# Performance work log

Measured on AMD Instinct MI355X. Metric: run time of the kernel, lower is better.

Reference implementation:

```python
import jax, jax.numpy as jnp
import numpy as np

LAMBDA = 0.01  # sparsity_threshold
SCALE = 0.02
NUM_BLOCKS = 4


def setup_inputs() -> dict:
    key = jax.random.key(0)
    k1, k2, k3, k4, k5 = jax.random.split(key, 5)
    B, N, C = 8, 4096, 512
    bs = C // NUM_BLOCKS
    return {
        "x": jax.random.normal(k1, (B, N, C), dtype=jnp.float32),
        "w1": jax.random.normal(k2, (2, NUM_BLOCKS, bs, bs), dtype=jnp.float32) * SCALE,
        "w2": jax.random.normal(k3, (2, NUM_BLOCKS, bs, bs), dtype=jnp.float32) * SCALE,
        "b1": jax.random.normal(k4, (2, NUM_BLOCKS, bs), dtype=jnp.float32) * SCALE,
        "b2": jax.random.normal(k5, (2, NUM_BLOCKS, bs), dtype=jnp.float32) * SCALE,
        "H": 64,
        "W": 64,
    }


def _softshrink(v):
    return jnp.where(v > LAMBDA, v - LAMBDA, jnp.where(v < -LAMBDA, v + LAMBDA, jnp.zeros((), v.dtype)))


def reference(x, w1, w2, b1, b2, H, W):
    B, N, C = x.shape
    bs = C // NUM_BLOCKS
    xb = x.reshape(B, N, NUM_BLOCKS, bs)
    # FFT over (token, block) axes, ortho norm — faithful to torch fft2(dim=(1,2))
    xf = jnp.fft.fft2(xb, axes=(1, 2), norm="ortho")
    re, im = jnp.real(xf), jnp.imag(xf)

    mul = lambda a, w: jnp.einsum("tnbd,bdk->tnbk", a, w)  # block-diagonal matmul

    r1 = jax.nn.relu(mul(re, w1[0]) - mul(im, w1[1]) + b1[0])
    i1 = jax.nn.relu(mul(re, w1[1]) + mul(im, w1[0]) + b1[1])
    r2 = mul(r1, w2[0]) - mul(i1, w2[1]) + b2[0]
    i2 = mul(r1, w2[1]) + mul(i1, w2[0]) + b2[1]

    z = _softshrink(r2) + 1j * _softshrink(i2)
    out = jnp.real(jnp.fft.ifft2(z, axes=(1, 2), norm="ortho"))  # .to(float32) keeps real part
    return out.reshape(B, N, C).astype(jnp.float32)
```

## Files before the change

### kernel.cpp

```cpp
#include <hip/hip_runtime.h>
#include <math.h>

#define TWO_PI 6.283185307179586f

typedef __attribute__((ext_vector_type(8))) short bf16x8;
typedef __attribute__((ext_vector_type(4))) short bf16x4;
typedef __attribute__((ext_vector_type(4))) float f32x4;
typedef __attribute__((ext_vector_type(4))) _Float16 h16x4;
typedef __attribute__((ext_vector_type(8))) _Float16 h16x8;

__device__ __forceinline__ short f2bf(float f) {
    unsigned u = __float_as_uint(f);
    unsigned r = (u + 0x7FFFu + ((u >> 16) & 1u)) >> 16;
    return (short)r;
}
__device__ __forceinline__ float bf2f(short s) {
    return __uint_as_float(((unsigned)(unsigned short)s) << 16);
}

__device__ __forceinline__ int dr4(int s) {
    return ((s & 3) << 4) | (s & 12) | ((s >> 4) & 3);
}

__device__ __forceinline__ void cmulw(float& xr, float& xi, float wr, float wi) {
    const float tr = xr * wr - xi * wi;
    xi = xr * wi + xi * wr;
    xr = tr;
}

template<int W>
__device__ __forceinline__ void fft64_dif4v(_Float16 (*Lre)[W], _Float16 (*Lim)[W],
                                            const float* wtr, const float* wti,
                                            int c4, int h) {
#pragma unroll
    for (int s = 0; s < 3; ++s) {
        const int q  = 16 >> (2 * s);
        const int tw = 1 << (2 * s);
        __syncthreads();
        const int j = h & (q - 1);
        const int g = (s == 0) ? 0 : (h >> (4 - 2 * s));
        const int i0 = g * (q << 2) + j;
        const int i1 = i0 + q, i2 = i1 + q, i3 = i2 + q;
        const h16x4 A0r = *(const h16x4*)&Lre[i0][c4], A0i = *(const h16x4*)&Lim[i0][c4];
        const h16x4 A1r = *(const h16x4*)&Lre[i1][c4], A1i = *(const h16x4*)&Lim[i1][c4];
        const h16x4 A2r = *(const h16x4*)&Lre[i2][c4], A2i = *(const h16x4*)&Lim[i2][c4];
        const h16x4 A3r = *(const h16x4*)&Lre[i3][c4], A3i = *(const h16x4*)&Lim[i3][c4];
        const int m = j * tw;
        const float w1r = wtr[m],     w1i = wti[m];
        const float w2r = wtr[2 * m], w2i = wti[2 * m];
        const float w3r = wtr[3 * m], w3i = wti[3 * m];
        h16x4 O0r, O0i, O1r, O1i, O2r, O2i, O3r, O3i;
#pragma unroll
        for (int e = 0; e < 4; ++e) {
            const float a0r = (float)A0r[e], a0i = (float)A0i[e];
            const float a1r = (float)A1r[e], a1i = (float)A1i[e];
            const float a2r = (float)A2r[e], a2i = (float)A2i[e];
            const float a3r = (float)A3r[e], a3i = (float)A3i[e];
            const float t0r = a0r + a2r, t0i = a0i + a2i;
            const float t2r = a0r - a2r, t2i = a0i - a2i;
            const float t1r = a1r + a3r, t1i = a1i + a3i;
            const float dr  = a1r - a3r, di  = a1i - a3i;
            const float t3r = di, t3i = -dr;
            O0r[e] = (_Float16)(t0r + t1r);  O0i[e] = (_Float16)(t0i + t1i);
            float y1r = t2r + t3r, y1i = t2i + t3i;
            float y2r = t0r - t1r, y2i = t0i - t1i;
            float y3r = t2r - t3r, y3i = t2i - t3i;
            if (m) {
                cmulw(y1r, y1i, w1r, w1i);
                cmulw(y2r, y2i, w2r, w2i);
                cmulw(y3r, y3i, w3r, w3i);
            }
            O1r[e] = (_Float16)y1r; O1i[e] = (_Float16)y1i;
            O2r[e] = (_Float16)y2r; O2i[e] = (_Float16)y2i;
            O3r[e] = (_Float16)y3r; O3i[e] = (_Float16)y3i;
        }
        *(h16x4*)&Lre[i0][c4] = O0r;  *(h16x4*)&Lim[i0][c4] = O0i;
        *(h16x4*)&Lre[i1][c4] = O1r;  *(h16x4*)&Lim[i1][c4] = O1i;
        *(h16x4*)&Lre[i2][c4] = O2r;  *(h16x4*)&Lim[i2][c4] = O2i;
        *(h16x4*)&Lre[i3][c4] = O3r;  *(h16x4*)&Lim[i3][c4] = O3i;
    }
    __syncthreads();
}

template<int W>
__device__ __forceinline__ void fft64_dit4v(_Float16 (*Lre)[W], _Float16 (*Lim)[W],
                                            const float* wtr, const float* wti,
                                            int c4, int h) {
#pragma unroll
    for (int s = 2; s >= 0; --s) {
        const int q  = 16 >> (2 * s);
        const int tw = 1 << (2 * s);
        __syncthreads();
        const int j = h & (q - 1);
        const int g = (s == 0) ? 0 : (h >> (4 - 2 * s));
        const int i0 = g * (q << 2) + j;
        const int i1 = i0 + q, i2 = i1 + q, i3 = i2 + q;
        const h16x4 A0r = *(const h16x4*)&Lre[i0][c4], A0i = *(const h16x4*)&Lim[i0][c4];
        const h16x4 A1r = *(const h16x4*)&Lre[i1][c4], A1i = *(const h16x4*)&Lim[i1][c4];
        const h16x4 A2r = *(const h16x4*)&Lre[i2][c4], A2i = *(const h16x4*)&Lim[i2][c4];
        const h16x4 A3r = *(const h16x4*)&Lre[i3][c4], A3i = *(const h16x4*)&Lim[i3][c4];
        const int m = j * tw;
        const float w1r = wtr[m],     w1i = -wti[m];
        const float w2r = wtr[2 * m], w2i = -wti[2 * m];
        const float w3r = wtr[3 * m], w3i = -wti[3 * m];
        h16x4 O0r, O0i, O1r, O1i, O2r, O2i, O3r, O3i;
#pragma unroll
        for (int e = 0; e < 4; ++e) {
            float b1r = (float)A1r[e], b1i = (float)A1i[e];
            float b2r = (float)A2r[e], b2i = (float)A2i[e];
            float b3r = (float)A3r[e], b3i = (float)A3i[e];
            if (m) {
                cmulw(b1r, b1i, w1r, w1i);
                cmulw(b2r, b2i, w2r, w2i);
                cmulw(b3r, b3i, w3r, w3i);
            }
            const float a0r = (float)A0r[e], a0i = (float)A0i[e];
            const float u0r = a0r + b2r, u0i = a0i + b2i;
            const float u1r = a0r - b2r, u1i = a0i - b2i;
            const float u2r = b1r + b3r, u2i = b1i + b3i;
            const float dr  = b1r - b3r, di  = b1i - b3i;
            const float u3r = -di, u3i = dr;
            O0r[e] = (_Float16)(u0r + u2r); O0i[e] = (_Float16)(u0i + u2i);
            O1r[e] = (_Float16)(u1r + u3r); O1i[e] = (_Float16)(u1i + u3i);
            O2r[e] = (_Float16)(u0r - u2r); O2i[e] = (_Float16)(u0i - u2i);
            O3r[e] = (_Float16)(u1r - u3r); O3i[e] = (_Float16)(u1i - u3i);
        }
        *(h16x4*)&Lre[i0][c4] = O0r;  *(h16x4*)&Lim[i0][c4] = O0i;
        *(h16x4*)&Lre[i1][c4] = O1r;  *(h16x4*)&Lim[i1][c4] = O1i;
        *(h16x4*)&Lre[i2][c4] = O2r;  *(h16x4*)&Lim[i2][c4] = O2i;
        *(h16x4*)&Lre[i3][c4] = O3r;  *(h16x4*)&Lim[i3][c4] = O3i;
    }
    __syncthreads();
}

#define DECODE_BCT() \
    const int b  = blockIdx.x >> 8; \
    const int dg = (blockIdx.x >> 2) & 63; \
    const int ct = blockIdx.x & 3;

#define GADDR(slot, blk, f4) \
    (((size_t)(b * 4096 + (slot)) * 512) + (size_t)((blk) * 128 + ct * 32 + (f4) * 4))

#define GADDR8(slot, blk, e8) \
    (((size_t)(b * 4096 + (slot)) * 512) + (size_t)((blk) * 128 + ct * 32 + (e8) * 8))

#define SETUP_TABLE48() \
    if (tid < 48) { \
        float s_, c_; \
        sincosf(TWO_PI * (float)tid / 64.0f, &s_, &c_); \
        wre[tid] = c_; wim[tid] = -s_; \
    }

extern "C" __global__ void __launch_bounds__(512)
fft_fwd_a(const float* __restrict__ x, short* __restrict__ zre, short* __restrict__ zim) {
    __shared__ __align__(16) _Float16 Lre[64][136];
    __shared__ __align__(16) _Float16 Lim[64][136];
    __shared__ float wre[48], wim[48];
    __shared__ float twr[64], twi[64];
    const int tid = threadIdx.x;
    SETUP_TABLE48();
    DECODE_BCT();
    if (tid >= 64 && tid < 128) {
        const int s1 = tid - 64;
        float sn, cs;
        sincosf(-(TWO_PI / 4096.0f) * (float)(dg * dr4(s1)), &sn, &cs);
        twr[s1] = cs; twi[s1] = sn;
    }
    for (int idx = tid; idx < 2048; idx += 512) {
        const int n1 = idx >> 5, q = idx & 31, blk = q >> 3, f4 = q & 7;
        const int cl = blk * 32 + f4 * 4;
        const float4 v = *(const float4*)(x + GADDR(n1 * 64 + dg, blk, f4));
        h16x4 hv, hz;
        hv[0] = (_Float16)v.x; hv[1] = (_Float16)v.y;
        hv[2] = (_Float16)v.z; hv[3] = (_Float16)v.w;
        hz[0] = (_Float16)0.f; hz[1] = (_Float16)0.f;
        hz[2] = (_Float16)0.f; hz[3] = (_Float16)0.f;
        *(h16x4*)&Lre[n1][cl] = hv;
        *(h16x4*)&Lim[n1][cl] = hz;
    }
    fft64_dif4v<136>(Lre, Lim, wre, wim, (tid & 31) * 4, tid >> 5);
    for (int idx = tid; idx < 2048; idx += 512) {
        const int s1 = idx >> 5, q = idx & 31, blk = q >> 3, f4 = q & 7;
        const int cl = blk * 32 + f4 * 4;
        const float cs = twr[s1], sn = twi[s1];
        const h16x4 hr = *(const h16x4*)&Lre[s1][cl];
        const h16x4 hi = *(const h16x4*)&Lim[s1][cl];
        bf16x4 pr, pi;
#pragma unroll
        for (int i = 0; i < 4; ++i) {
            const float vr = (float)hr[i], vi = (float)hi[i];
            pr[i] = f2bf(vr * cs - vi * sn);
            pi[i] = f2bf(vr * sn + vi * cs);
        }
        const size_t g = GADDR(s1 * 64 + dg, blk, f4);
        *(bf16x4*)(zre + g) = pr;
        *(bf16x4*)(zim + g) = pi;
    }
}

extern "C" __global__ void __launch_bounds__(512)
fft_fwd_b(short* __restrict__ zre, short* __restrict__ zim) {
    __shared__ __align__(16) _Float16 Lre[64][136];
    __shared__ __align__(16) _Float16 Lim[64][136];
    __shared__ float wre[48], wim[48];
    const int tid = threadIdx.x;
    SETUP_TABLE48();
    DECODE_BCT();
    for (int idx = tid; idx < 1024; idx += 512) {
        const int n2 = idx >> 4, q = idx & 15, blk = q >> 2, e8 = q & 3;
        const int cl = blk * 32 + e8 * 8;
        const size_t g = GADDR8(dg * 64 + n2, blk, e8);
        const bf16x8 vr = *(const bf16x8*)(zre + g);
        const bf16x8 vi = *(const bf16x8*)(zim + g);
        h16x8 hr, hi;
#pragma unroll
        for (int i = 0; i < 8; ++i) {
            hr[i] = (_Float16)bf2f(vr[i]);
            hi[i] = (_Float16)bf2f(vi[i]);
        }
        *(h16x8*)&Lre[n2][cl] = hr;
        *(h16x8*)&Lim[n2][cl] = hi;
    }
    fft64_dif4v<136>(Lre, Lim, wre, wim, (tid & 31) * 4, tid >> 5);
    {
        const int s = tid >> 3, dq = tid & 7;
        const int cb = dq * 4;
        h16x4 R[4], M[4];
#pragma unroll
        for (int qq = 0; qq < 4; ++qq) {
            R[qq] = *(const h16x4*)&Lre[s][cb + qq * 32];
            M[qq] = *(const h16x4*)&Lim[s][cb + qq * 32];
        }
        h16x4 YR[4], YM[4];
        const float sc = 1.0f / 128.0f;
#pragma unroll
        for (int e = 0; e < 4; ++e) {
            const float r0 = (float)R[0][e], r1 = (float)R[1][e];
            const float r2 = (float)R[2][e], r3 = (float)R[3][e];
            const float m0 = (float)M[0][e], m1 = (float)M[1][e];
            const float m2 = (float)M[2][e], m3 = (float)M[3][e];
            YR[0][e] = (_Float16)((r0 + r1 + r2 + r3) * sc);
            YM[0][e] = (_Float16)((m0 + m1 + m2 + m3) * sc);
            YR[1][e] = (_Float16)((r0 + m1 - r2 - m3) * sc);
            YM[1][e] = (_Float16)((m0 - r1 - m2 + r3) * sc);
            YR[2][e] = (_Float16)((r0 - r1 + r2 - r3) * sc);
            YM[2][e] = (_Float16)((m0 - m1 + m2 - m3) * sc);
            YR[3][e] = (_Float16)((r0 - m1 - r2 + m3) * sc);
            YM[3][e] = (_Float16)((m0 + r1 - m2 - r3) * sc);
        }
#pragma unroll
        for (int qq = 0; qq < 4; ++qq) {
            *(h16x4*)&Lre[s][cb + qq * 32] = YR[qq];
            *(h16x4*)&Lim[s][cb + qq * 32] = YM[qq];
        }
    }
    __syncthreads();
    for (int idx = tid; idx < 1024; idx += 512) {
        const int s2 = idx >> 4, q = idx & 15, blk = q >> 2, e8 = q & 3;
        const int cl = blk * 32 + e8 * 8;
        const h16x8 hr = *(const h16x8*)&Lre[s2][cl];
        const h16x8 hi = *(const h16x8*)&Lim[s2][cl];
        bf16x8 pr, pi;
#pragma unroll
        for (int i = 0; i < 8; ++i) {
            pr[i] = f2bf((float)hr[i]);
            pi[i] = f2bf((float)hi[i]);
        }
        const size_t g = GADDR8(dg * 64 + s2, blk, e8);
        *(bf16x8*)(zre + g) = pr;
        *(bf16x8*)(zim + g) = pi;
    }
}

extern "C" __global__ void __launch_bounds__(512)
fft_inv_a(short* __restrict__ zre, short* __restrict__ zim) {
    __shared__ __align__(16) _Float16 Lre[64][136];
    __shared__ __align__(16) _Float16 Lim[64][136];
    __shared__ float wre[48], wim[48];
    __shared__ float twr[64], twi[64];
    const int tid = threadIdx.x;
    SETUP_TABLE48();
    DECODE_BCT();
    if (tid >= 64 && tid < 128) {
        const int n2 = tid - 64;
        float sn, cs;
        sincosf((TWO_PI / 4096.0f) * (float)(n2 * dr4(dg)), &sn, &cs);
        twr[n2] = cs; twi[n2] = sn;
    }
    for (int idx = tid; idx < 1024; idx += 512) {
        const int s2 = idx >> 4, q = idx & 15, blk = q >> 2, e8 = q & 3;
        const int cl = blk * 32 + e8 * 8;
        const size_t g = GADDR8(dg * 64 + s2, blk, e8);
        const bf16x8 vr = *(const bf16x8*)(zre + g);
        const bf16x8 vi = *(const bf16x8*)(zim + g);
        h16x8 hr, hi;
#pragma unroll
        for (int i = 0; i < 8; ++i) {
            hr[i] = (_Float16)bf2f(vr[i]);
            hi[i] = (_Float16)bf2f(vi[i]);
        }
        *(h16x8*)&Lre[s2][cl] = hr;
        *(h16x8*)&Lim[s2][cl] = hi;
    }
    __syncthreads();
    {
        const int s = tid >> 3, dq = tid & 7;
        const int cb = dq * 4;
        h16x4 R[4], M[4];
#pragma unroll
        for (int qq = 0; qq < 4; ++qq) {
            R[qq] = *(const h16x4*)&Lre[s][cb + qq * 32];
            M[qq] = *(const h16x4*)&Lim[s][cb + qq * 32];
        }
        h16x4 YR[4], YM[4];
        const float sc = 1.0f / 128.0f;
#pragma unroll
        for (int e = 0; e < 4; ++e) {
            const float r0 = (float)R[0][e], r1 = (float)R[1][e];
            const float r2 = (float)R[2][e], r3 = (float)R[3][e];
            const float m0 = (float)M[0][e], m1 = (float)M[1][e];
            const float m2 = (float)M[2][e], m3 = (float)M[3][e];
            YR[0][e] = (_Float16)((r0 + r1 + r2 + r3) * sc);
            YM[0][e] = (_Float16)((m0 + m1 + m2 + m3) * sc);
            YR[1][e] = (_Float16)((r0 - m1 - r2 + m3) * sc);
            YM[1][e] = (_Float16)((m0 + r1 - m2 - r3) * sc);
            YR[2][e] = (_Float16)((r0 - r1 + r2 - r3) * sc);
            YM[2][e] = (_Float16)((m0 - m1 + m2 - m3) * sc);
            YR[3][e] = (_Float16)((r0 + m1 - r2 - m3) * sc);
            YM[3][e] = (_Float16)((m0 - r1 - m2 + r3) * sc);
        }
#pragma unroll
        for (int qq = 0; qq < 4; ++qq) {
            *(h16x4*)&Lre[s][cb + qq * 32] = YR[qq];
            *(h16x4*)&Lim[s][cb + qq * 32] = YM[qq];
        }
    }
    fft64_dit4v<136>(Lre, Lim, wre, wim, (tid & 31) * 4, tid >> 5);
    for (int idx = tid; idx < 2048; idx += 512) {
        const int n2 = idx >> 5, q = idx & 31, blk = q >> 3, f4 = q & 7;
        const int cl = blk * 32 + f4 * 4;
        const float cs = twr[n2], sn = twi[n2];
        const h16x4 hr = *(const h16x4*)&Lre[n2][cl];
        const h16x4 hi = *(const h16x4*)&Lim[n2][cl];
        bf16x4 pr, pi;
#pragma unroll
        for (int i = 0; i < 4; ++i) {
            const float vr = (float)hr[i], vi = (float)hi[i];
            pr[i] = f2bf(vr * cs - vi * sn);
            pi[i] = f2bf(vr * sn + vi * cs);
        }
        const size_t g = GADDR(dg * 64 + n2, blk, f4);
        *(bf16x4*)(zre + g) = pr;
        *(bf16x4*)(zim + g) = pi;
    }
}

extern "C" __global__ void __launch_bounds__(512)
fft_inv_b(const short* __restrict__ zre, const short* __restrict__ zim,
          float* __restrict__ out) {
    __shared__ __align__(16) _Float16 Lre[64][136];
    __shared__ __align__(16) _Float16 Lim[64][136];
    __shared__ float wre[48], wim[48];
    const int tid = threadIdx.x;
    SETUP_TABLE48();
    DECODE_BCT();
    for (int idx = tid; idx < 1024; idx += 512) {
        const int s1 = idx >> 4, q = idx & 15, blk = q >> 2, e8 = q & 3;
        const int cl = blk * 32 + e8 * 8;
        const size_t g = GADDR8(s1 * 64 + dg, blk, e8);
        const bf16x8 vr = *(const bf16x8*)(zre + g);
        const bf16x8 vi = *(const bf16x8*)(zim + g);
        h16x8 hr, hi;
#pragma unroll
        for (int i = 0; i < 8; ++i) {
            hr[i] = (_Float16)bf2f(vr[i]);
            hi[i] = (_Float16)bf2f(vi[i]);
        }
        *(h16x8*)&Lre[s1][cl] = hr;
        *(h16x8*)&Lim[s1][cl] = hi;
    }
    fft64_dit4v<136>(Lre, Lim, wre, wim, (tid & 31) * 4, tid >> 5);
    for (int idx = tid; idx < 2048; idx += 512) {
        const int n1 = idx >> 5, q = idx & 31, blk = q >> 3, f4 = q & 7;
        const int cl = blk * 32 + f4 * 4;
        const h16x4 hr = *(const h16x4*)&Lre[n1][cl];
        float4 o;
        o.x = (float)hr[0]; o.y = (float)hr[1];
        o.z = (float)hr[2]; o.w = (float)hr[3];
        *(float4*)(out + GADDR(n1 * 64 + dg, blk, f4)) = o;
    }
}

extern "C" __global__ void __launch_bounds__(256)
wprep(const float* __restrict__ w1, const float* __restrict__ w2,
      short* __restrict__ wb) {
    const int i4  = blockIdx.x * 256 + threadIdx.x;
    const int k0  = (i4 & 63) * 4;
    const int n   = (i4 >> 6) & 255;
    const int blk = (i4 >> 14) & 3;
    const int L   = i4 >> 16;
    const float* w = L ? w2 : w1;
    bf16x4 pv;
#pragma unroll
    for (int j = 0; j < 4; ++j) {
        const int k = k0 + j;
        float v;
        if (k < 128) {
            v = (n < 128) ? w[blk * 16384 + k * 128 + n]
                          : w[65536 + blk * 16384 + k * 128 + (n - 128)];
        } else {
            v = (n < 128) ? -w[65536 + blk * 16384 + (k - 128) * 128 + n]
                          :  w[blk * 16384 + (k - 128) * 128 + (n - 128)];
        }
        pv[j] = f2bf(v);
    }
    *(bf16x4*)(wb + (size_t)i4 * 4) = pv;
}

#define MITER 4

__device__ __forceinline__ void stage_tile(const short* __restrict__ zre,
                                           const short* __restrict__ zim,
                                           char* Abuf, int rowbase, int blk,
                                           int wave, int lane) {
#pragma unroll
    for (int it = 0; it < 4; ++it) {
        const int chunk = wave * 256 + it * 64 + lane;
        const int row   = chunk >> 5;
        const unsigned kbyte = ((unsigned)((chunk & 31) << 4)) ^ ((unsigned)((row & 7) << 4));
        const int k0 = (int)(kbyte >> 1);
        const short* src = (k0 < 128) ? zre : zim;
        const size_t g = (size_t)(rowbase + row) * 512 + blk * 128 + (k0 & 127);
        unsigned* lp = (unsigned*)(Abuf + (wave * 4096 + it * 1024));
        __builtin_amdgcn_global_load_lds((const unsigned*)(src + g), lp, 16, 0, 0);
    }
}

template<int LAYER>
__global__ void __launch_bounds__(512)
mlp_mfma(short* __restrict__ zre, short* __restrict__ zim,
         const short* __restrict__ wb, const float* __restrict__ bias) {
    __shared__ __align__(16) char As[2][64 * 256 * 2];

    const int blk  = blockIdx.y;
    const int tid  = threadIdx.x;
    const int wave = tid >> 6;
    const int lane = tid & 63;
    const int lrow = lane & 15;
    const int lk   = lane >> 4;

    bf16x8 Bf[2][8];
#pragma unroll
    for (int nt = 0; nt < 2; ++nt) {
        const int n = wave * 32 + nt * 16 + lrow;
#pragma unroll
        for (int ks = 0; ks < 8; ++ks) {
            Bf[nt][ks] = *(const bf16x8*)(wb + ((size_t)(blk * 256 + n) * 256 + ks * 32 + lk * 8));
        }
    }

    float bv[2];
#pragma unroll
    for (int nt = 0; nt < 2; ++nt) {
        const int n = wave * 32 + nt * 16 + lrow;
        bv[nt] = (n < 128) ? bias[blk * 128 + n] : bias[512 + blk * 128 + (n - 128)];
    }

    stage_tile(zre, zim, As[0], blockIdx.x * MITER * 64, blk, wave, lane);

    for (int t = 0; t < MITER; ++t) {
        __syncthreads();

        if (t + 1 < MITER)
            stage_tile(zre, zim, As[(t + 1) & 1],
                       (blockIdx.x * MITER + t + 1) * 64, blk, wave, lane);

        const char* Ab = As[t & 1];
        const int rowbase = (blockIdx.x * MITER + t) * 64;

        f32x4 acc[4][2];
#pragma unroll
        for (int mt = 0; mt < 4; ++mt)
#pragma unroll
            for (int nt = 0; nt < 2; ++nt)
                acc[mt][nt] = (f32x4){0.f, 0.f, 0.f, 0.f};

#pragma unroll
        for (int ks = 0; ks < 8; ++ks) {
            bf16x8 af[4];
#pragma unroll
            for (int mt = 0; mt < 4; ++mt) {
                const int row = mt * 16 + lrow;
                const int k0  = ks * 32 + lk * 8;
                const unsigned byteoff =
                    ((unsigned)(row * 512 + k0 * 2)) ^ ((unsigned)((row & 7) << 4));
                af[mt] = *(const bf16x8*)(Ab + byteoff);
            }
#pragma unroll
            for (int mt = 0; mt < 4; ++mt)
#pragma unroll
                for (int nt = 0; nt < 2; ++nt)
                    acc[mt][nt] = __builtin_amdgcn_mfma_f32_16x16x32_bf16(
                        af[mt], Bf[nt][ks], acc[mt][nt], 0, 0, 0);
        }

#pragma unroll
        for (int nt = 0; nt < 2; ++nt) {
            const int n = wave * 32 + nt * 16 + lrow;
            short* dst = (n < 128) ? zre : zim;
            const int col = blk * 128 + (n & 127);
#pragma unroll
            for (int mt = 0; mt < 4; ++mt) {
#pragma unroll
                for (int r = 0; r < 4; ++r) {
                    const int row = rowbase + mt * 16 + lk * 4 + r;
                    float v = acc[mt][nt][r] + bv[nt];
                    if (LAYER == 1) {
                        v = fmaxf(v, 0.0f);
                    } else {
                        v = (v > 0.01f) ? v - 0.01f : ((v < -0.01f) ? v + 0.01f : 0.0f);
                    }
                    dst[(size_t)row * 512 + col] = f2bf(v);
                }
            }
        }
    }
}

extern "C" void kernel_launch(void* const* d_in, const int* in_sizes, int n_in,
                              void* d_out, int out_size, void* d_ws, size_t ws_size,
                              hipStream_t stream) {
    const float* x  = (const float*)d_in[0];
    const float* w1 = (const float*)d_in[1];
    const float* w2 = (const float*)d_in[2];
    const float* b1 = (const float*)d_in[3];
    const float* b2 = (const float*)d_in[4];

    float* out = (float*)d_out;
    short* zre = (short*)d_ws;
    short* zim = zre + 16777216;
    short* wb  = (short*)d_out;
    const size_t WB_L = 4ull * 256 * 256;

    wprep<<<512, 256, 0, stream>>>(w1, w2, wb);

    fft_fwd_a<<<2048, 512, 0, stream>>>(x, zre, zim);
    fft_fwd_b<<<2048, 512, 0, stream>>>(zre, zim);

    mlp_mfma<1><<<dim3(32768 / (64 * MITER), 4), 512, 0, stream>>>(zre, zim, wb, b1);
    mlp_mfma<2><<<dim3(32768 / (64 * MITER), 4), 512, 0, stream>>>(zre, zim, wb + WB_L, b2);

    fft_inv_a<<<2048, 512, 0, stream>>>(zre, zim);
    fft_inv_b<<<2048, 512, 0, stream>>>(zre, zim, out);
}
```

Baseline: 221.3 us.

## Double-buffer async global-to-LDS loads in middle FFT kernels with bf16 swizzled tiles

fft_fwd_b and fft_inv_a now keep their tiles in LDS as bf16 with an XOR swizzle, loaded through global_load_lds. Each block processes four batch elements in a loop and prefetches the next tile into a second buffer while it computes the current one. The grid for these kernels shrinks accordingly, and the fp16 conversion passes are dropped. This aims to hide global load latency and cut conversion work, at the cost of fewer blocks, extra barriers and bf16 rounding between FFT stages.

```diff
diff --git a/kernel.cpp b/kernel.cpp
--- a/kernel.cpp
+++ b/kernel.cpp
@@ -28,109 +28,131 @@
     xr = tr;
 }
 
-template<int W>
-__device__ __forceinline__ void fft64_dif4v(_Float16 (*Lre)[W], _Float16 (*Lim)[W],
-                                            const float* wtr, const float* wti,
-                                            int c4, int h) {
-#pragma unroll
-    for (int s = 0; s < 3; ++s) {
-        const int q  = 16 >> (2 * s);
-        const int tw = 1 << (2 * s);
-        __syncthreads();
-        const int j = h & (q - 1);
-        const int g = (s == 0) ? 0 : (h >> (4 - 2 * s));
-        const int i0 = g * (q << 2) + j;
-        const int i1 = i0 + q, i2 = i1 + q, i3 = i2 + q;
-        const h16x4 A0r = *(const h16x4*)&Lre[i0][c4], A0i = *(const h16x4*)&Lim[i0][c4];
-        const h16x4 A1r = *(const h16x4*)&Lre[i1][c4], A1i = *(const h16x4*)&Lim[i1][c4];
-        const h16x4 A2r = *(const h16x4*)&Lre[i2][c4], A2i = *(const h16x4*)&Lim[i2][c4];
-        const h16x4 A3r = *(const h16x4*)&Lre[i3][c4], A3i = *(const h16x4*)&Lim[i3][c4];
-        const int m = j * tw;
-        const float w1r = wtr[m],     w1i = wti[m];
-        const float w2r = wtr[2 * m], w2i = wti[2 * m];
-        const float w3r = wtr[3 * m], w3i = wti[3 * m];
-        h16x4 O0r, O0i, O1r, O1i, O2r, O2i, O3r, O3i;
-#pragma unroll
-        for (int e = 0; e < 4; ++e) {
-            const float a0r = (float)A0r[e], a0i = (float)A0i[e];
-            const float a1r = (float)A1r[e], a1i = (float)A1i[e];
-            const float a2r = (float)A2r[e], a2i = (float)A2i[e];
-            const float a3r = (float)A3r[e], a3i = (float)A3i[e];
-            const float t0r = a0r + a2r, t0i = a0i + a2i;
-            const float t2r = a0r - a2r, t2i = a0i - a2i;
-            const float t1r = a1r + a3r, t1i = a1i + a3i;
-            const float dr  = a1r - a3r, di  = a1i - a3i;
-            const float t3r = di, t3i = -dr;
-            O0r[e] = (_Float16)(t0r + t1r);  O0i[e] = (_Float16)(t0i + t1i);
-            float y1r = t2r + t3r, y1i = t2i + t3i;
-            float y2r = t0r - t1r, y2i = t0i - t1i;
-            float y3r = t2r - t3r, y3i = t2i - t3i;
-            if (m) {
-                cmulw(y1r, y1i, w1r, w1i);
-                cmulw(y2r, y2i, w2r, w2i);
-                cmulw(y3r, y3i, w3r, w3i);
-            }
-            O1r[e] = (_Float16)y1r; O1i[e] = (_Float16)y1i;
-            O2r[e] = (_Float16)y2r; O2i[e] = (_Float16)y2i;
-            O3r[e] = (_Float16)y3r; O3i[e] = (_Float16)y3i;
-        }
-        *(h16x4*)&Lre[i0][c4] = O0r;  *(h16x4*)&Lim[i0][c4] = O0i;
-        *(h16x4*)&Lre[i1][c4] = O1r;  *(h16x4*)&Lim[i1][c4] = O1i;
-        *(h16x4*)&Lre[i2][c4] = O2r;  *(h16x4*)&Lim[i2][c4] = O2i;
-        *(h16x4*)&Lre[i3][c4] = O3r;  *(h16x4*)&Lim[i3][c4] = O3i;
-    }
-    __syncthreads();
-}
-
-template<int W>
-__device__ __forceinline__ void fft64_dit4v(_Float16 (*Lre)[W], _Float16 (*Lim)[W],
-                                            const float* wtr, const float* wti,
-                                            int c4, int h) {
-#pragma unroll
-    for (int s = 2; s >= 0; --s) {
-        const int q  = 16 >> (2 * s);
-        const int tw = 1 << (2 * s);
-        __syncthreads();
-        const int j = h & (q - 1);
-        const int g = (s == 0) ? 0 : (h >> (4 - 2 * s));
-        const int i0 = g * (q << 2) + j;
-        const int i1 = i0 + q, i2 = i1 + q, i3 = i2 + q;
-        const h16x4 A0r = *(const h16x4*)&Lre[i0][c4], A0i = *(const h16x4*)&Lim[i0][c4];
-        const h16x4 A1r = *(const h16x4*)&Lre[i1][c4], A1i = *(const h16x4*)&Lim[i1][c4];
-        const h16x4 A2r = *(const h16x4*)&Lre[i2][c4], A2i = *(const h16x4*)&Lim[i2][c4];
-        const h16x4 A3r = *(const h16x4*)&Lre[i3][c4], A3i = *(const h16x4*)&Lim[i3][c4];
-        const int m = j * tw;
-        const float w1r = wtr[m],     w1i = -wti[m];
-        const float w2r = wtr[2 * m], w2i = -wti[2 * m];
-        const float w3r = wtr[3 * m], w3i = -wti[3 * m];
-        h16x4 O0r, O0i, O1r, O1i, O2r, O2i, O3r, O3i;
-#pragma unroll
-        for (int e = 0; e < 4; ++e) {
-            float b1r = (float)A1r[e], b1i = (float)A1i[e];
-            float b2r = (float)A2r[e], b2i = (float)A2i[e];
-            float b3r = (float)A3r[e], b3i = (float)A3i[e];
-            if (m) {
-                cmulw(b1r, b1i, w1r, w1i);
-                cmulw(b2r, b2i, w2r, w2i);
-                cmulw(b3r, b3i, w3r, w3i);
-            }
-            const float a0r = (float)A0r[e], a0i = (float)A0i[e];
-            const float u0r = a0r + b2r, u0i = a0i + b2i;
-            const float u1r = a0r - b2r, u1i = a0i - b2i;
-            const float u2r = b1r + b3r, u2i = b1i + b3i;
-            const float dr  = b1r - b3r, di  = b1i - b3i;
-            const float u3r = -di, u3i = dr;
-            O0r[e] = (_Float16)(u0r + u2r); O0i[e] = (_Float16)(u0i + u2i);
-            O1r[e] = (_Float16)(u1r + u3r); O1i[e] = (_Float16)(u1i + u3i);
-            O2r[e] = (_Float16)(u0r - u2r); O2i[e] = (_Float16)(u0i - u2i);
-            O3r[e] = (_Float16)(u1r - u3r); O3i[e] = (_Float16)(u1i - u3i);
-        }
-        *(h16x4*)&Lre[i0][c4] = O0r;  *(h16x4*)&Lim[i0][c4] = O0i;
-        *(h16x4*)&Lre[i1][c4] = O1r;  *(h16x4*)&Lim[i1][c4] = O1i;
-        *(h16x4*)&Lre[i2][c4] = O2r;  *(h16x4*)&Lim[i2][c4] = O2i;
-        *(h16x4*)&Lre[i3][c4] = O3r;  *(h16x4*)&Lim[i3][c4] = O3i;
-    }
-    __syncthreads();
+__device__ __forceinline__ f32x4 ld4bf(const char* Z, int off) {
+    const bf16x4 v = *(const bf16x4*)(Z + off);
+    f32x4 r;
+    r[0] = bf2f(v[0]); r[1] = bf2f(v[1]); r[2] = bf2f(v[2]); r[3] = bf2f(v[3]);
+    return r;
+}
+__device__ __forceinline__ void st4bf(char* Z, int off, f32x4 a) {
+    bf16x4 v;
+    v[0] = f2bf(a[0]); v[1] = f2bf(a[1]); v[2] = f2bf(a[2]); v[3] = f2bf(a[3]);
+    *(bf16x4*)(Z + off) = v;
+}
+
+__device__ __forceinline__ int swzoff(int r, int cb) {
+    return r * 256 + (cb ^ ((r & 7) << 4));
+}
+
+__device__ __forceinline__ void dif_stage_bf(char* Z, const float* wtr, const float* wti,
+                                             int cb, int h, int s) {
+    const int q  = 16 >> (2 * s);
+    const int tw = 1 << (2 * s);
+    const int j = h & (q - 1);
+    const int g = (s == 0) ? 0 : (h >> (4 - 2 * s));
+    const int i0 = g * (q << 2) + j;
+    const int i1 = i0 + q, i2 = i1 + q, i3 = i2 + q;
+    const int o0 = swzoff(i0, cb), o1 = swzoff(i1, cb);
+    const int o2 = swzoff(i2, cb), o3 = swzoff(i3, cb);
+    const f32x4 a0r = ld4bf(Z, o0), a0i = ld4bf(Z + 16384, o0);
+    const f32x4 a1r = ld4bf(Z, o1), a1i = ld4bf(Z + 16384, o1);
+    const f32x4 a2r = ld4bf(Z, o2), a2i = ld4bf(Z + 16384, o2);
+    const f32x4 a3r = ld4bf(Z, o3), a3i = ld4bf(Z + 16384, o3);
+    const int m = j * tw;
+    const float w1r = wtr[m],     w1i = wti[m];
+    const float w2r = wtr[2 * m], w2i = wti[2 * m];
+    const float w3r = wtr[3 * m], w3i = wti[3 * m];
+    f32x4 O0r, O0i, O1r, O1i, O2r, O2i, O3r, O3i;
+#pragma unroll
+    for (int e = 0; e < 4; ++e) {
+        const float t0r = a0r[e] + a2r[e], t0i = a0i[e] + a2i[e];
+        const float t2r = a0r[e] - a2r[e], t2i = a0i[e] - a2i[e];
+        const float t1r = a1r[e] + a3r[e], t1i = a1i[e] + a3i[e];
+        const float dr  = a1r[e] - a3r[e], di  = a1i[e] - a3i[e];
+        const float t3r = di, t3i = -dr;
+        O0r[e] = t0r + t1r;  O0i[e] = t0i + t1i;
+        float y1r = t2r + t3r, y1i = t2i + t3i;
+        float y2r = t0r - t1r, y2i = t0i - t1i;
+        float y3r = t2r - t3r, y3i = t2i - t3i;
+        if (m) {
+            cmulw(y1r, y1i, w1r, w1i);
+            cmulw(y2r, y2i, w2r, w2i);
+            cmulw(y3r, y3i, w3r, w3i);
+        }
+        O1r[e] = y1r; O1i[e] = y1i;
+        O2r[e] = y2r; O2i[e] = y2i;
+        O3r[e] = y3r; O3i[e] = y3i;
+    }
+    st4bf(Z, o0, O0r);  st4bf(Z + 16384, o0, O0i);
+    st4bf(Z, o1, O1r);  st4bf(Z + 16384, o1, O1i);
+    st4bf(Z, o2, O2r);  st4bf(Z + 16384, o2, O2i);
+    st4bf(Z, o3, O3r);  st4bf(Z + 16384, o3, O3i);
+}
+
+__device__ __forceinline__ void dit_stage_bf(char* Z, const float* wtr, const float* wti,
+                                             int cb, int h, int s) {
+    const int q  = 16 >> (2 * s);
+    const int tw = 1 << (2 * s);
+    const int j = h & (q - 1);
+    const int g = (s == 0) ? 0 : (h >> (4 - 2 * s));
+    const int i0 = g * (q << 2) + j;
+    const int i1 = i0 + q, i2 = i1 + q, i3 = i2 + q;
+    const int o0 = swzoff(i0, cb), o1 = swzoff(i1, cb);
+    const int o2 = swzoff(i2, cb), o3 = swzoff(i3, cb);
+    const f32x4 a0r = ld4bf(Z, o0), a0i = ld4bf(Z + 16384, o0);
+    const f32x4 a1r = ld4bf(Z, o1), a1i = ld4bf(Z + 16384, o1);
+    const f32x4 a2r = ld4bf(Z, o2), a2i = ld4bf(Z + 16384, o2);
+    const f32x4 a3r = ld4bf(Z, o3), a3i = ld4bf(Z + 16384, o3);
+    const int m = j * tw;
+    const float w1r = wtr[m],     w1i = -wti[m];
+    const float w2r = wtr[2 * m], w2i = -wti[2 * m];
+    const float w3r = wtr[3 * m], w3i = -wti[3 * m];
+    f32x4 O0r, O0i, O1r, O1i, O2r, O2i, O3r, O3i;
+#pragma unroll
+    for (int e = 0; e < 4; ++e) {
+        float b1r = a1r[e], b1i = a1i[e];
+        float b2r = a2r[e], b2i = a2i[e];
+        float b3r = a3r[e], b3i = a3i[e];
+        if (m) {
+            cmulw(b1r, b1i, w1r, w1i);
+            cmulw(b2r, b2i, w2r, w2i);
+            cmulw(b3r, b3i, w3r, w3i);
+        }
+        const float u0r = a0r[e] + b2r, u0i = a0i[e] + b2i;
+        const float u1r = a0r[e] - b2r, u1i = a0i[e] - b2i;
+        const float u2r = b1r + b3r,    u2i = b1i + b3i;
+        const float dr  = b1r - b3r,    di  = b1i - b3i;
+        const float u3r = -di, u3i = dr;
+        O0r[e] = u0r + u2r; O0i[e] = u0i + u2i;
+        O1r[e] = u1r + u3r; O1i[e] = u1i + u3i;
+        O2r[e] = u0r - u2r; O2i[e] = u0i - u2i;
+        O3r[e] = u1r - u3r; O3i[e] = u1i - u3i;
+    }
+    st4bf(Z, o0, O0r);  st4bf(Z + 16384, o0, O0i);
+    st4bf(Z, o1, O1r);  st4bf(Z + 16384, o1, O1i);
+    st4bf(Z, o2, O2r);  st4bf(Z + 16384, o2, O2i);
+    st4bf(Z, o3, O3r);  st4bf(Z + 16384, o3, O3i);
+}
+
+__device__ __forceinline__ void stage_ztile(const short* __restrict__ zre,
+                                            const short* __restrict__ zim,
+                                            char* Zbuf, int b, int dg, int ct,
+                                            int wave, int lane) {
+#pragma unroll
+    for (int it = 0; it < 4; ++it) {
+        const int q = wave * 256 + it * 64 + lane;
+        const int p = q >> 10;
+        const int r = q & 1023;
+        const int slot = r >> 4;
+        const int c = r & 15;
+        const int c_log = c ^ (slot & 7);
+        const int blk = c_log >> 2, cj = c_log & 3;
+        const short* src = p ? zim : zre;
+        const size_t g = ((size_t)(b * 4096 + dg * 64 + slot) * 512)
+                       + (size_t)(blk * 128 + ct * 32 + cj * 8);
+        unsigned* lp = (unsigned*)(Zbuf + (wave * 4096 + it * 1024));
+        __builtin_amdgcn_global_load_lds((const unsigned*)(src + g), lp, 16, 0, 0);
+    }
 }
 
 #define DECODE_BCT() \
@@ -178,7 +200,58 @@
         *(h16x4*)&Lre[n1][cl] = hv;
         *(h16x4*)&Lim[n1][cl] = hz;
     }
-    fft64_dif4v<136>(Lre, Lim, wre, wim, (tid & 31) * 4, tid >> 5);
+    {
+        const int c4 = (tid & 31) * 4;
+        const int h = tid >> 5;
+#pragma unroll
+        for (int s = 0; s < 3; ++s) {
+            const int q  = 16 >> (2 * s);
+            const int tw = 1 << (2 * s);
+            __syncthreads();
+            const int j = h & (q - 1);
+            const int g = (s == 0) ? 0 : (h >> (4 - 2 * s));
+            const int i0 = g * (q << 2) + j;
+            const int i1 = i0 + q, i2 = i1 + q, i3 = i2 + q;
+            const h16x4 A0r = *(const h16x4*)&Lre[i0][c4], A0i = *(const h16x4*)&Lim[i0][c4];
+            const h16x4 A1r = *(const h16x4*)&Lre[i1][c4], A1i = *(const h16x4*)&Lim[i1][c4];
+            const h16x4 A2r = *(const h16x4*)&Lre[i2][c4], A2i = *(const h16x4*)&Lim[i2][c4];
+            const h16x4 A3r = *(const h16x4*)&Lre[i3][c4], A3i = *(const h16x4*)&Lim[i3][c4];
+            const int m = j * tw;
+            const float w1r = wre[m],     w1i = wim[m];
+            const float w2r = wre[2 * m], w2i = wim[2 * m];
+            const float w3r = wre[3 * m], w3i = wim[3 * m];
+            h16x4 O0r, O0i, O1r, O1i, O2r, O2i, O3r, O3i;
+#pragma unroll
+            for (int e = 0; e < 4; ++e) {
+                const float a0r = (float)A0r[e], a0i = (float)A0i[e];
+                const float a1r = (float)A1r[e], a1i = (float)A1i[e];
+                const float a2r = (float)A2r[e], a2i = (float)A2i[e];
+                const float a3r = (float)A3r[e], a3i = (float)A3i[e];
+                const float t0r = a0r + a2r, t0i = a0i + a2i;
+                const float t2r = a0r - a2r, t2i = a0i - a2i;
+                const float t1r = a1r + a3r, t1i = a1i + a3i;
+                const float dr  = a1r - a3r, di  = a1i - a3i;
+                const float t3r = di, t3i = -dr;
+                O0r[e] = (_Float16)(t0r + t1r);  O0i[e] = (_Float16)(t0i + t1i);
+                float y1r = t2r + t3r, y1i = t2i + t3i;
+                float y2r = t0r - t1r, y2i = t0i - t1i;
+                float y3r = t2r - t3r, y3i = t2i - t3i;
+                if (m) {
+                    cmulw(y1r, y1i, w1r, w1i);
+                    cmulw(y2r, y2i, w2r, w2i);
+                    cmulw(y3r, y3i, w3r, w3i);
+                }
+                O1r[e] = (_Float16)y1r; O1i[e] = (_Float16)y1i;
+                O2r[e] = (_Float16)y2r; O2i[e] = (_Float16)y2i;
+                O3r[e] = (_Float16)y3r; O3i[e] = (_Float16)y3i;
+            }
+            *(h16x4*)&Lre[i0][c4] = O0r;  *(h16x4*)&Lim[i0][c4] = O0i;
+            *(h16x4*)&Lre[i1][c4] = O1r;  *(h16x4*)&Lim[i1][c4] = O1i;
+            *(h16x4*)&Lre[i2][c4] = O2r;  *(h16x4*)&Lim[i2][c4] = O2i;
+            *(h16x4*)&Lre[i3][c4] = O3r;  *(h16x4*)&Lim[i3][c4] = O3i;
+        }
+        __syncthreads();
+    }
     for (int idx = tid; idx < 2048; idx += 512) {
         const int s1 = idx >> 5, q = idx & 31, blk = q >> 3, f4 = q & 7;
         const int cl = blk * 32 + f4 * 4;
@@ -200,158 +273,169 @@
 
 extern "C" __global__ void __launch_bounds__(512)
 fft_fwd_b(short* __restrict__ zre, short* __restrict__ zim) {
-    __shared__ __align__(16) _Float16 Lre[64][136];
-    __shared__ __align__(16) _Float16 Lim[64][136];
+    __shared__ __align__(16) char Zs[2][32768];
     __shared__ float wre[48], wim[48];
     const int tid = threadIdx.x;
     SETUP_TABLE48();
-    DECODE_BCT();
-    for (int idx = tid; idx < 1024; idx += 512) {
-        const int n2 = idx >> 4, q = idx & 15, blk = q >> 2, e8 = q & 3;
-        const int cl = blk * 32 + e8 * 8;
-        const size_t g = GADDR8(dg * 64 + n2, blk, e8);
-        const bf16x8 vr = *(const bf16x8*)(zre + g);
-        const bf16x8 vi = *(const bf16x8*)(zim + g);
-        h16x8 hr, hi;
-#pragma unroll
-        for (int i = 0; i < 8; ++i) {
-            hr[i] = (_Float16)bf2f(vr[i]);
-            hi[i] = (_Float16)bf2f(vi[i]);
-        }
-        *(h16x8*)&Lre[n2][cl] = hr;
-        *(h16x8*)&Lim[n2][cl] = hi;
-    }
-    fft64_dif4v<136>(Lre, Lim, wre, wim, (tid & 31) * 4, tid >> 5);
-    {
-        const int s = tid >> 3, dq = tid & 7;
-        const int cb = dq * 4;
-        h16x4 R[4], M[4];
-#pragma unroll
-        for (int qq = 0; qq < 4; ++qq) {
-            R[qq] = *(const h16x4*)&Lre[s][cb + qq * 32];
-            M[qq] = *(const h16x4*)&Lim[s][cb + qq * 32];
-        }
-        h16x4 YR[4], YM[4];
-        const float sc = 1.0f / 128.0f;
-#pragma unroll
-        for (int e = 0; e < 4; ++e) {
-            const float r0 = (float)R[0][e], r1 = (float)R[1][e];
-            const float r2 = (float)R[2][e], r3 = (float)R[3][e];
-            const float m0 = (float)M[0][e], m1 = (float)M[1][e];
-            const float m2 = (float)M[2][e], m3 = (float)M[3][e];
-            YR[0][e] = (_Float16)((r0 + r1 + r2 + r3) * sc);
-            YM[0][e] = (_Float16)((m0 + m1 + m2 + m3) * sc);
-            YR[1][e] = (_Float16)((r0 + m1 - r2 - m3) * sc);
-            YM[1][e] = (_Float16)((m0 - r1 - m2 + r3) * sc);
-            YR[2][e] = (_Float16)((r0 - r1 + r2 - r3) * sc);
-            YM[2][e] = (_Float16)((m0 - m1 + m2 - m3) * sc);
-            YR[3][e] = (_Float16)((r0 - m1 - r2 + m3) * sc);
-            YM[3][e] = (_Float16)((m0 + r1 - m2 - r3) * sc);
-        }
-#pragma unroll
-        for (int qq = 0; qq < 4; ++qq) {
-            *(h16x4*)&Lre[s][cb + qq * 32] = YR[qq];
-            *(h16x4*)&Lim[s][cb + qq * 32] = YM[qq];
-        }
-    }
-    __syncthreads();
-    for (int idx = tid; idx < 1024; idx += 512) {
-        const int s2 = idx >> 4, q = idx & 15, blk = q >> 2, e8 = q & 3;
-        const int cl = blk * 32 + e8 * 8;
-        const h16x8 hr = *(const h16x8*)&Lre[s2][cl];
-        const h16x8 hi = *(const h16x8*)&Lim[s2][cl];
-        bf16x8 pr, pi;
-#pragma unroll
-        for (int i = 0; i < 8; ++i) {
-            pr[i] = f2bf((float)hr[i]);
-            pi[i] = f2bf((float)hi[i]);
-        }
-        const size_t g = GADDR8(dg * 64 + s2, blk, e8);
-        *(bf16x8*)(zre + g) = pr;
-        *(bf16x8*)(zim + g) = pi;
+    const int bh = blockIdx.x >> 8;
+    const int dg = (blockIdx.x >> 2) & 63;
+    const int ct = blockIdx.x & 3;
+    const int wave = tid >> 6, lane = tid & 63;
+    const int cb = (tid & 31) * 8;
+    const int h  = tid >> 5;
+
+    stage_ztile(zre, zim, Zs[0], bh * 4, dg, ct, wave, lane);
+
+    for (int t = 0; t < 4; ++t) {
+        __syncthreads();
+        if (t + 1 < 4)
+            stage_ztile(zre, zim, Zs[(t + 1) & 1], bh * 4 + t + 1, dg, ct, wave, lane);
+
+        char* Z = Zs[t & 1];
+        dif_stage_bf(Z, wre, wim, cb, h, 0);
+        __syncthreads();
+        dif_stage_bf(Z, wre, wim, cb, h, 1);
+        __syncthreads();
+        dif_stage_bf(Z, wre, wim, cb, h, 2);
+        __syncthreads();
+
+        {
+            const int slot = tid >> 3, jg4 = tid & 7;
+            const int jb = jg4 * 8;
+            f32x4 r[4], m[4];
+#pragma unroll
+            for (int b4 = 0; b4 < 4; ++b4) {
+                const int off = swzoff(slot, b4 * 64 + jb);
+                r[b4] = ld4bf(Z, off);
+                m[b4] = ld4bf(Z + 16384, off);
+            }
+            const float sc = 1.0f / 128.0f;
+            f32x4 yr[4], ym[4];
+#pragma unroll
+            for (int e = 0; e < 4; ++e) {
+                const float r0 = r[0][e], r1 = r[1][e], r2 = r[2][e], r3 = r[3][e];
+                const float m0 = m[0][e], m1 = m[1][e], m2 = m[2][e], m3 = m[3][e];
+                yr[0][e] = (r0 + r1 + r2 + r3) * sc;  ym[0][e] = (m0 + m1 + m2 + m3) * sc;
+                yr[1][e] = (r0 + m1 - r2 - m3) * sc;  ym[1][e] = (m0 - r1 - m2 + r3) * sc;
+                yr[2][e] = (r0 - r1 + r2 - r3) * sc;  ym[2][e] = (m0 - m1 + m2 - m3) * sc;
+                yr[3][e] = (r0 - m1 - r2 + m3) * sc;  ym[3][e] = (m0 + r1 - m2 - r3) * sc;
+            }
+#pragma unroll
+            for (int b4 = 0; b4 < 4; ++b4) {
+                const int off = swzoff(slot, b4 * 64 + jb);
+                st4bf(Z, off, yr[b4]);
+                st4bf(Z + 16384, off, ym[b4]);
+            }
+        }
+        __syncthreads();
+
+        const int b = bh * 4 + t;
+#pragma unroll
+        for (int kq = 0; kq < 4; ++kq) {
+            const int q = wave * 256 + kq * 64 + lane;
+            const int p = q >> 10;
+            const int r2 = q & 1023;
+            const int slot = r2 >> 4;
+            const int c = r2 & 15;
+            const int c_log = c ^ (slot & 7);
+            const int blk = c_log >> 2, cj = c_log & 3;
+            const bf16x8 v = *(const bf16x8*)(Z + q * 16);
+            short* dst = p ? zim : zre;
+            const size_t g = ((size_t)(b * 4096 + dg * 64 + slot) * 512)
+                           + (size_t)(blk * 128 + ct * 32 + cj * 8);
+            *(bf16x8*)(dst + g) = v;
+        }
     }
 }
 
 extern "C" __global__ void __launch_bounds__(512)
 fft_inv_a(short* __restrict__ zre, short* __restrict__ zim) {
-    __shared__ __align__(16) _Float16 Lre[64][136];
-    __shared__ __align__(16) _Float16 Lim[64][136];
+    __shared__ __align__(16) char Zs[2][32768];
     __shared__ float wre[48], wim[48];
     __shared__ float twr[64], twi[64];
     const int tid = threadIdx.x;
     SETUP_TABLE48();
-    DECODE_BCT();
+    const int bh = blockIdx.x >> 8;
+    const int dg = (blockIdx.x >> 2) & 63;
+    const int ct = blockIdx.x & 3;
     if (tid >= 64 && tid < 128) {
         const int n2 = tid - 64;
         float sn, cs;
         sincosf((TWO_PI / 4096.0f) * (float)(n2 * dr4(dg)), &sn, &cs);
         twr[n2] = cs; twi[n2] = sn;
     }
-    for (int idx = tid; idx < 1024; idx += 512) {
-        const int s2 = idx >> 4, q = idx & 15, blk = q >> 2, e8 = q & 3;
-        const int cl = blk * 32 + e8 * 8;
-        const size_t g = GADDR8(dg * 64 + s2, blk, e8);
-        const bf16x8 vr = *(const bf16x8*)(zre + g);
-        const bf16x8 vi = *(const bf16x8*)(zim + g);
-        h16x8 hr, hi;
-#pragma unroll
-        for (int i = 0; i < 8; ++i) {
-            hr[i] = (_Float16)bf2f(vr[i]);
-            hi[i] = (_Float16)bf2f(vi[i]);
-        }
-        *(h16x8*)&Lre[s2][cl] = hr;
-        *(h16x8*)&Lim[s2][cl] = hi;
-    }
-    __syncthreads();
-    {
-        const int s = tid >> 3, dq = tid & 7;
-        const int cb = dq * 4;
-        h16x4 R[4], M[4];
-#pragma unroll
-        for (int qq = 0; qq < 4; ++qq) {
-            R[qq] = *(const h16x4*)&Lre[s][cb + qq * 32];
-            M[qq] = *(const h16x4*)&Lim[s][cb + qq * 32];
-        }
-        h16x4 YR[4], YM[4];
-        const float sc = 1.0f / 128.0f;
-#pragma unroll
-        for (int e = 0; e < 4; ++e) {
-            const float r0 = (float)R[0][e], r1 = (float)R[1][e];
-            const float r2 = (float)R[2][e], r3 = (float)R[3][e];
-            const float m0 = (float)M[0][e], m1 = (float)M[1][e];
-            const float m2 = (float)M[2][e], m3 = (float)M[3][e];
-            YR[0][e] = (_Float16)((r0 + r1 + r2 + r3) * sc);
-            YM[0][e] = (_Float16)((m0 + m1 + m2 + m3) * sc);
-            YR[1][e] = (_Float16)((r0 - m1 - r2 + m3) * sc);
-            YM[1][e] = (_Float16)((m0 + r1 - m2 - r3) * sc);
-            YR[2][e] = (_Float16)((r0 - r1 + r2 - r3) * sc);
-            YM[2][e] = (_Float16)((m0 - m1 + m2 - m3) * sc);
-            YR[3][e] = (_Float16)((r0 + m1 - r2 - m3) * sc);
-            YM[3][e] = (_Float16)((m0 - r1 - m2 + r3) * sc);
-        }
-#pragma unroll
-        for (int qq = 0; qq < 4; ++qq) {
-            *(h16x4*)&Lre[s][cb + qq * 32] = YR[qq];
-            *(h16x4*)&Lim[s][cb + qq * 32] = YM[qq];
-        }
-    }
-    fft64_dit4v<136>(Lre, Lim, wre, wim, (tid & 31) * 4, tid >> 5);
-    for (int idx = tid; idx < 2048; idx += 512) {
-        const int n2 = idx >> 5, q = idx & 31, blk = q >> 3, f4 = q & 7;
-        const int cl = blk * 32 + f4 * 4;
-        const float cs = twr[n2], sn = twi[n2];
-        const h16x4 hr = *(const h16x4*)&Lre[n2][cl];
-        const h16x4 hi = *(const h16x4*)&Lim[n2][cl];
-        bf16x4 pr, pi;
-#pragma unroll
-        for (int i = 0; i < 4; ++i) {
-            const float vr = (float)hr[i], vi = (float)hi[i];
-            pr[i] = f2bf(vr * cs - vi * sn);
-            pi[i] = f2bf(vr * sn + vi * cs);
-        }
-        const size_t g = GADDR(dg * 64 + n2, blk, f4);
-        *(bf16x4*)(zre + g) = pr;
-        *(bf16x4*)(zim + g) = pi;
+    const int wave = tid >> 6, lane = tid & 63;
+    const int cb = (tid & 31) * 8;
+    const int h  = tid >> 5;
+
+    stage_ztile(zre, zim, Zs[0], bh * 4, dg, ct, wave, lane);
+
+    for (int t = 0; t < 4; ++t) {
+        __syncthreads();
+        if (t + 1 < 4)
+            stage_ztile(zre, zim, Zs[(t + 1) & 1], bh * 4 + t + 1, dg, ct, wave, lane);
+
+        char* Z = Zs[t & 1];
+
+        {
+            const int slot = tid >> 3, jg4 = tid & 7;
+            const int jb = jg4 * 8;
+            f32x4 r[4], m[4];
+#pragma unroll
+            for (int b4 = 0; b4 < 4; ++b4) {
+                const int off = swzoff(slot, b4 * 64 + jb);
+                r[b4] = ld4bf(Z, off);
+                m[b4] = ld4bf(Z + 16384, off);
+            }
+            const float sc = 1.0f / 128.0f;
+            f32x4 yr[4], ym[4];
+#pragma unroll
+            for (int e = 0; e < 4; ++e) {
+                const float r0 = r[0][e], r1 = r[1][e], r2 = r[2][e], r3 = r[3][e];
+                const float m0 = m[0][e], m1 = m[1][e], m2 = m[2][e], m3 = m[3][e];
+                yr[0][e] = (r0 + r1 + r2 + r3) * sc;  ym[0][e] = (m0 + m1 + m2 + m3) * sc;
+                yr[1][e] = (r0 - m1 - r2 + m3) * sc;  ym[1][e] = (m0 + r1 - m2 - r3) * sc;
+                yr[2][e] = (r0 - r1 + r2 - r3) * sc;  ym[2][e] = (m0 - m1 + m2 - m3) * sc;
+                yr[3][e] = (r0 + m1 - r2 - m3) * sc;  ym[3][e] = (m0 - r1 - m2 + r3) * sc;
+            }
+#pragma unroll
+            for (int b4 = 0; b4 < 4; ++b4) {
+                const int off = swzoff(slot, b4 * 64 + jb);
+                st4bf(Z, off, yr[b4]);
+                st4bf(Z + 16384, off, ym[b4]);
+            }
+        }
+        __syncthreads();
+        dit_stage_bf(Z, wre, wim, cb, h, 2);
+        __syncthreads();
+        dit_stage_bf(Z, wre, wim, cb, h, 1);
+        __syncthreads();
+        dit_stage_bf(Z, wre, wim, cb, h, 0);
+        __syncthreads();
+
+        const int b = bh * 4 + t;
+#pragma unroll
+        for (int k = 0; k < 2; ++k) {
+            const int idx = tid + k * 512;
+            const int slot = idx >> 4;
+            const int c = idx & 15;
+            const int c_log = c ^ (slot & 7);
+            const int blk = c_log >> 2, cj = c_log & 3;
+            const bf16x8 vr = *(const bf16x8*)(Z + slot * 256 + c * 16);
+            const bf16x8 vi = *(const bf16x8*)(Z + 16384 + slot * 256 + c * 16);
+            const float cs = twr[slot], sn = twi[slot];
+            bf16x8 pr, pi;
+#pragma unroll
+            for (int i = 0; i < 8; ++i) {
+                const float ar = bf2f(vr[i]), ai = bf2f(vi[i]);
+                pr[i] = f2bf(ar * cs - ai * sn);
+                pi[i] = f2bf(ar * sn + ai * cs);
+            }
+            const size_t g = ((size_t)(b * 4096 + dg * 64 + slot) * 512)
+                           + (size_t)(blk * 128 + ct * 32 + cj * 8);
+            *(bf16x8*)(zre + g) = pr;
+            *(bf16x8*)(zim + g) = pi;
+        }
     }
 }
 
@@ -379,7 +463,55 @@
         *(h16x8*)&Lre[s1][cl] = hr;
         *(h16x8*)&Lim[s1][cl] = hi;
     }
-    fft64_dit4v<136>(Lre, Lim, wre, wim, (tid & 31) * 4, tid >> 5);
+    {
+        const int c4 = (tid & 31) * 4;
+        const int h = tid >> 5;
+#pragma unroll
+        for (int s = 2; s >= 0; --s) {
+            const int q  = 16 >> (2 * s);
+            const int tw = 1 << (2 * s);
+            __syncthreads();
+            const int j = h & (q - 1);
+            const int g = (s == 0) ? 0 : (h >> (4 - 2 * s));
+            const int i0 = g * (q << 2) + j;
+            const int i1 = i0 + q, i2 = i1 + q, i3 = i2 + q;
+            const h16x4 A0r = *(const h16x4*)&Lre[i0][c4], A0i = *(const h16x4*)&Lim[i0][c4];
+            const h16x4 A1r = *(const h16x4*)&Lre[i1][c4], A1i = *(const h16x4*)&Lim[i1][c4];
+            const h16x4 A2r = *(const h16x4*)&Lre[i2][c4], A2i = *(const h16x4*)&Lim[i2][c4];
+            const h16x4 A3r = *(const h16x4*)&Lre[i3][c4], A3i = *(const h16x4*)&Lim[i3][c4];
+            const int m = j * tw;
+            const float w1r = wre[m],     w1i = -wim[m];
+            const float w2r = wre[2 * m], w2i = -wim[2 * m];
+            const float w3r = wre[3 * m], w3i = -wim[3 * m];
+            h16x4 O0r, O0i, O1r, O1i, O2r, O2i, O3r, O3i;
+#pragma unroll
+            for (int e = 0; e < 4; ++e) {
+                float b1r = (float)A1r[e], b1i = (float)A1i[e];
+                float b2r = (float)A2r[e], b2i = (float)A2i[e];
+                float b3r = (float)A3r[e], b3i = (float)A3i[e];
+                if (m) {
+                    cmulw(b1r, b1i, w1r, w1i);
+                    cmulw(b2r, b2i, w2r, w2i);
+                    cmulw(b3r, b3i, w3r, w3i);
+                }
+                const float a0r = (float)A0r[e], a0i = (float)A0i[e];
+                const float u0r = a0r + b2r, u0i = a0i + b2i;
+                const float u1r = a0r - b2r, u1i = a0i - b2i;
+                const float u2r = b1r + b3r, u2i = b1i + b3i;
+                const float dr  = b1r - b3r, di  = b1i - b3i;
+                const float u3r = -di, u3i = dr;
+                O0r[e] = (_Float16)(u0r + u2r); O0i[e] = (_Float16)(u0i + u2i);
+                O1r[e] = (_Float16)(u1r + u3r); O1i[e] = (_Float16)(u1i + u3i);
+                O2r[e] = (_Float16)(u0r - u2r); O2i[e] = (_Float16)(u0i - u2i);
+                O3r[e] = (_Float16)(u1r - u3r); O3i[e] = (_Float16)(u1i - u3i);
+            }
+            *(h16x4*)&Lre[i0][c4] = O0r;  *(h16x4*)&Lim[i0][c4] = O0i;
+            *(h16x4*)&Lre[i1][c4] = O1r;  *(h16x4*)&Lim[i1][c4] = O1i;
+            *(h16x4*)&Lre[i2][c4] = O2r;  *(h16x4*)&Lim[i2][c4] = O2i;
+            *(h16x4*)&Lre[i3][c4] = O3r;  *(h16x4*)&Lim[i3][c4] = O3i;
+        }
+        __syncthreads();
+    }
     for (int idx = tid; idx < 2048; idx += 512) {
         const int n1 = idx >> 5, q = idx & 31, blk = q >> 3, f4 = q & 7;
         const int cl = blk * 32 + f4 * 4;
@@ -545,11 +677,11 @@
     wprep<<<512, 256, 0, stream>>>(w1, w2, wb);
 
     fft_fwd_a<<<2048, 512, 0, stream>>>(x, zre, zim);
-    fft_fwd_b<<<2048, 512, 0, stream>>>(zre, zim);
+    fft_fwd_b<<<512, 512, 0, stream>>>(zre, zim);
 
     mlp_mfma<1><<<dim3(32768 / (64 * MITER), 4), 512, 0, stream>>>(zre, zim, wb, b1);
     mlp_mfma<2><<<dim3(32768 / (64 * MITER), 4), 512, 0, stream>>>(zre, zim, wb + WB_L, b2);
 
-    fft_inv_a<<<2048, 512, 0, stream>>>(zre, zim);
+    fft_inv_a<<<512, 512, 0, stream>>>(zre, zim);
     fft_inv_b<<<2048, 512, 0, stream>>>(zre, zim, out);
 }
```

Result: slower. 235.3 us (+6.3%).
